# Kernel tuning notes

Hardware: AMD Instinct MI355X
Metric: run time of the kernel (lower is better)

## Reference

```python
import jax, jax.numpy as jnp
import numpy as np

NUM_HEADING_BIN = 12
NUM_SIZE_CLUSTER = 8
DELTA_NORM_W = 0.01
CENTER_W = 0.5
B, N = 4096, 2048


def huber(err, delta=1.0):
    a = jnp.abs(err)
    q = jnp.minimum(a, delta)
    return jnp.mean(0.5 * q * q + delta * (a - q))


def box3d_corners(centers, headings, sizes):
    # centers (B,3), headings (B,), sizes (B,3) -> (B,8,3)
    l, w, h = sizes[:, 0:1], sizes[:, 1:2], sizes[:, 2:3]
    sx = jnp.asarray([1, 1, -1, -1, 1, 1, -1, -1], dtype=sizes.dtype)
    sy = jnp.asarray([1, -1, -1, 1, 1, -1, -1, 1], dtype=sizes.dtype)
    sz = jnp.asarray([1, 1, 1, 1, -1, -1, -1, -1], dtype=sizes.dtype)
    corners = jnp.stack([0.5 * l * sx, 0.5 * w * sy, 0.5 * h * sz], axis=1)  # (B,3,8)
    c, s = jnp.cos(headings), jnp.sin(headings)
    z, o = jnp.zeros_like(c), jnp.ones_like(c)
    R = jnp.stack([jnp.stack([c, -s, z], -1),
                   jnp.stack([s, c, z], -1),
                   jnp.stack([z, z, o], -1)], axis=1)  # (B,3,3)
    out = jnp.einsum('bij,bjk->bik', R, corners) + centers[:, :, None]
    return jnp.transpose(out, (0, 2, 1))  # (B,8,3)


def setup_inputs() -> dict:
    key = jax.random.key(0)
    ks = jax.random.split(key, 9)
    return {
        'mask_xyz_mean': jax.random.normal(ks[0], (B, 3), jnp.float32),
        'point_cloud': jax.random.normal(ks[1], (B, 3, N), jnp.float32),
        'x_delta': jax.random.normal(ks[2], (B, 3, N), jnp.float32),
        'center_label': jax.random.normal(ks[3], (B, 3), jnp.float32),
        'size_residual_label': jax.random.normal(ks[4], (B, 3), jnp.float32),
        'heading_residual_label': jax.random.normal(ks[5], (B,), jnp.float32),
        'mean_sizes': jax.random.uniform(ks[6], (NUM_SIZE_CLUSTER, 3), jnp.float32, 0.5, 2.5),
        'size_class_label': jax.random.randint(ks[7], (B,), 0, NUM_SIZE_CLUSTER, jnp.int32),
        'heading_class_label': jax.random.randint(ks[8], (B,), 0, NUM_HEADING_BIN, jnp.int32),
    }


def reference(mask_xyz_mean, point_cloud, x_delta, center_label,
              size_residual_label, heading_residual_label, mean_sizes,
              size_class_label, heading_class_label):
    eps = 0.0  # faithful: original has no eps
    # center loss
    center_dist = jnp.linalg.norm(mask_xyz_mean - center_label, axis=1)
    center_loss = CENTER_W * huber(center_dist)

    # label assembly (onehot-sum == gather)
    size_label = mean_sizes[size_class_label] + size_residual_label  # (B,3)
    bin_centers = jnp.arange(0, np.pi, np.pi / NUM_HEADING_BIN, dtype=jnp.float32)
    heading_label = heading_residual_label + bin_centers[heading_class_label]  # (B,)

    corners_3d_gt = box3d_corners(center_label, heading_label, size_label)
    corners_2d_gt = corners_3d_gt[:, 4:8, :2]  # (B,4,2)

    v = center_label[:, :2]  # (B,2)
    p_dir = jnp.stack([-v[:, 1], v[:, 0]], axis=1)
    p_dir = p_dir / jnp.linalg.norm(p_dir, axis=1, keepdims=True)  # (B,2)

    pp_label = jnp.einsum('bkc,bc->bk', corners_2d_gt, p_dir)  # (B,4)
    py_max, py_min = jnp.max(pp_label, axis=1), jnp.min(pp_label, axis=1)
    std_y_label = (py_max - py_min) / 4
    mean_y_label = (py_max + py_min) / 2

    v_norm = jnp.linalg.norm(v, axis=1, keepdims=True)  # (B,1)
    proj_label = jnp.einsum('bkc,bc->bk', corners_2d_gt, v) / v_norm  # (B,4)
    p_max, p_min = jnp.max(proj_label, axis=1), jnp.min(proj_label, axis=1)
    std_label = (p_max - p_min) / 4
    mean_label = (p_max + p_min) / 2

    pc_xy = jnp.transpose(point_cloud, (0, 2, 1))[:, :, :2]  # (B,N,2)

    pp_pc = jnp.einsum('bnc,bc->bn', pc_xy, p_dir)  # (B,N)
    std_y_pc = jnp.std(pp_pc, axis=1, ddof=1)
    mean_y_pc = jnp.mean(pp_pc, axis=1)
    y_std_loss = huber(jnp.abs(std_y_label - std_y_pc))
    y_mean_loss = huber(jnp.abs(mean_y_label - mean_y_pc))

    proj_pc = jnp.einsum('bnc,bc->bn', pc_xy, v) / v_norm  # (B,N)
    std_pc = jnp.std(proj_pc, axis=1, ddof=1)
    mean_pc = jnp.mean(proj_pc, axis=1)
    x_std_loss = huber(jnp.abs(std_label - std_pc))
    x_mean_loss = huber(jnp.abs(mean_label - mean_pc))

    delta_norm = jnp.sqrt(jnp.sum(x_delta * x_delta, axis=(1, 2)))
    delta_norm_loss = DELTA_NORM_W * huber(delta_norm)

    total = center_loss + x_std_loss + x_mean_loss + delta_norm_loss + y_mean_loss + y_std_loss
    return 0.4 * total
```

## Files before the change

kernel.cpp:

```cpp
#include <hip/hip_runtime.h>
#include <math.h>

#define B_SZ 4096
#define N_PTS 2048
#define BLOCK 256

__device__ __forceinline__ float huber1(float a) {
    float q = fminf(a, 1.0f);
    return 0.5f * q * q + (a - q);
}

__global__ __launch_bounds__(BLOCK) void loss_stage1(
    const float* __restrict__ mask_xyz_mean,
    const float* __restrict__ point_cloud,
    const float* __restrict__ x_delta,
    const float* __restrict__ center_label,
    const float* __restrict__ size_residual,
    const float* __restrict__ heading_residual,
    const float* __restrict__ mean_sizes,
    const int*   __restrict__ size_class,
    const int*   __restrict__ heading_class,
    float* __restrict__ ws)
{
    const int b   = blockIdx.x;
    const int tid = threadIdx.x;

    const float cx = center_label[b * 3 + 0];
    const float cy = center_label[b * 3 + 1];

    const float vnorm2 = cx * cx + cy * cy;
    const float vnorm  = sqrtf(vnorm2);
    const float pdx = -cy / vnorm;
    const float pdy =  cx / vnorm;

    const size_t base = (size_t)b * 3 * N_PTS;
    const float4* px4 = (const float4*)(point_cloud + base);
    const float4* py4 = (const float4*)(point_cloud + base + N_PTS);
    const float4* pd4 = (const float4*)(x_delta + base);

    float s_pp = 0.f, s_pp2 = 0.f, s_t = 0.f, s_t2 = 0.f, s_d2 = 0.f;

    #pragma unroll
    for (int k = 0; k < N_PTS / 4 / BLOCK; ++k) {
        const int i = tid + k * BLOCK;
        const float4 x4 = px4[i];
        const float4 y4 = py4[i];
        {
            float pp = x4.x * pdx + y4.x * pdy;
            float t  = x4.x * cx  + y4.x * cy;
            s_pp += pp; s_pp2 += pp * pp; s_t += t; s_t2 += t * t;
        }
        {
            float pp = x4.y * pdx + y4.y * pdy;
            float t  = x4.y * cx  + y4.y * cy;
            s_pp += pp; s_pp2 += pp * pp; s_t += t; s_t2 += t * t;
        }
        {
            float pp = x4.z * pdx + y4.z * pdy;
            float t  = x4.z * cx  + y4.z * cy;
            s_pp += pp; s_pp2 += pp * pp; s_t += t; s_t2 += t * t;
        }
        {
            float pp = x4.w * pdx + y4.w * pdy;
            float t  = x4.w * cx  + y4.w * cy;
            s_pp += pp; s_pp2 += pp * pp; s_t += t; s_t2 += t * t;
        }
    }

    #pragma unroll
    for (int k = 0; k < 3 * N_PTS / 4 / BLOCK; ++k) {
        const int i = tid + k * BLOCK;
        const float4 d = pd4[i];
        s_d2 += d.x * d.x + d.y * d.y + d.z * d.z + d.w * d.w;
    }

    #pragma unroll
    for (int off = 32; off > 0; off >>= 1) {
        s_pp  += __shfl_down(s_pp,  off, 64);
        s_pp2 += __shfl_down(s_pp2, off, 64);
        s_t   += __shfl_down(s_t,   off, 64);
        s_t2  += __shfl_down(s_t2,  off, 64);
        s_d2  += __shfl_down(s_d2,  off, 64);
    }

    __shared__ float red[BLOCK / 64][5];
    const int wave = tid >> 6;
    const int lane = tid & 63;
    if (lane == 0) {
        red[wave][0] = s_pp;  red[wave][1] = s_pp2;
        red[wave][2] = s_t;   red[wave][3] = s_t2;
        red[wave][4] = s_d2;
    }
    __syncthreads();

    if (tid == 0) {
        #pragma unroll
        for (int w = 1; w < BLOCK / 64; ++w) {
            s_pp  += red[w][0];
            s_pp2 += red[w][1];
            s_t   += red[w][2];
            s_t2  += red[w][3];
            s_d2  += red[w][4];
        }

        const float mx = mask_xyz_mean[b * 3 + 0];
        const float my = mask_xyz_mean[b * 3 + 1];
        const float mz = mask_xyz_mean[b * 3 + 2];
        const float cz = center_label[b * 3 + 2];
        const float dxc = mx - cx, dyc = my - cy, dzc = mz - cz;
        const float center_dist = sqrtf(dxc * dxc + dyc * dyc + dzc * dzc);

        const int sc = size_class[b];
        const float l  = mean_sizes[sc * 3 + 0] + size_residual[b * 3 + 0];
        const float w_ = mean_sizes[sc * 3 + 1] + size_residual[b * 3 + 1];

        const float theta = heading_residual[b] +
                            (float)heading_class[b] * (float)(M_PI / 12.0);
        const float c = cosf(theta);
        const float s = sinf(theta);
        const float hl = 0.5f * l, hw = 0.5f * w_;

        float X[4], Y[4];
        X[0] =  c * hl - s * hw + cx;  Y[0] =  s * hl + c * hw + cy;
        X[1] =  c * hl + s * hw + cx;  Y[1] =  s * hl - c * hw + cy;
        X[2] = -c * hl + s * hw + cx;  Y[2] = -s * hl - c * hw + cy;
        X[3] = -c * hl - s * hw + cx;  Y[3] = -s * hl + c * hw + cy;

        float ppmax = -INFINITY, ppmin = INFINITY;
        float pmax  = -INFINITY, pmin  = INFINITY;
        #pragma unroll
        for (int k = 0; k < 4; ++k) {
            const float pp = X[k] * pdx + Y[k] * pdy;
            const float pj = (X[k] * cx + Y[k] * cy) / vnorm;
            ppmax = fmaxf(ppmax, pp); ppmin = fminf(ppmin, pp);
            pmax  = fmaxf(pmax,  pj); pmin  = fminf(pmin,  pj);
        }
        const float std_y_label  = (ppmax - ppmin) * 0.25f;
        const float mean_y_label = (ppmax + ppmin) * 0.5f;
        const float std_label    = (pmax - pmin) * 0.25f;
        const float mean_label   = (pmax + pmin) * 0.5f;

        const float invN   = 1.0f / (float)N_PTS;
        const float invNm1 = 1.0f / (float)(N_PTS - 1);

        const float mean_y_pc = s_pp * invN;
        const float var_y = (s_pp2 - s_pp * s_pp * invN) * invNm1;
        const float std_y_pc = sqrtf(fmaxf(var_y, 0.0f));

        const float mean_pc = (s_t * invN) / vnorm;
        const float var_x = ((s_t2 - s_t * s_t * invN) * invNm1) / vnorm2;
        const float std_pc = sqrtf(fmaxf(var_x, 0.0f));

        const float delta_norm = sqrtf(s_d2);

        const float total =
              0.5f  * huber1(center_dist)
            +         huber1(fabsf(std_label  - std_pc))
            +         huber1(fabsf(mean_label - mean_pc))
            + 0.01f * huber1(delta_norm)
            +         huber1(fabsf(mean_y_label - mean_y_pc))
            +         huber1(fabsf(std_y_label  - std_y_pc));

        ws[b] = total;
    }
}

__global__ __launch_bounds__(BLOCK) void loss_stage2(
    const float* __restrict__ ws, float* __restrict__ out)
{
    const int tid = threadIdx.x;
    const float4* w4 = (const float4*)ws;

    float s = 0.f;
    #pragma unroll
    for (int k = 0; k < B_SZ / 4 / BLOCK; ++k) {
        const float4 v = w4[tid + k * BLOCK];
        s += v.x + v.y + v.z + v.w;
    }

    #pragma unroll
    for (int off = 32; off > 0; off >>= 1)
        s += __shfl_down(s, off, 64);

    __shared__ float red[BLOCK / 64];
    const int wave = tid >> 6;
    const int lane = tid & 63;
    if (lane == 0) red[wave] = s;
    __syncthreads();

    if (tid == 0) {
        #pragma unroll
        for (int w = 1; w < BLOCK / 64; ++w) s += red[w];
        out[0] = s * (0.4f / (float)B_SZ);
    }
}

extern "C" void kernel_launch(void* const* d_in, const int* in_sizes, int n_in,
                              void* d_out, int out_size, void* d_ws, size_t ws_size,
                              hipStream_t stream) {
    const float* mask_xyz_mean    = (const float*)d_in[0];
    const float* point_cloud      = (const float*)d_in[1];
    const float* x_delta          = (const float*)d_in[2];
    const float* center_label     = (const float*)d_in[3];
    const float* size_residual    = (const float*)d_in[4];
    const float* heading_residual = (const float*)d_in[5];
    const float* mean_sizes       = (const float*)d_in[6];
    const int*   size_class       = (const int*)d_in[7];
    const int*   heading_class    = (const int*)d_in[8];
    float* ws  = (float*)d_ws;
    float* out = (float*)d_out;

    loss_stage1<<<B_SZ, BLOCK, 0, stream>>>(
        mask_xyz_mean, point_cloud, x_delta, center_label, size_residual,
        heading_residual, mean_sizes, size_class, heading_class, ws);
    loss_stage2<<<1, BLOCK, 0, stream>>>(ws, out);
}
```

Before: 221.6 us.

## Split per-batch reduction into two block roles and parallelize per-batch epilogue

Stage 1 now launches two blocks per batch element: one reduces point-cloud projections, the other reduces the squared norm of x_delta, so each block does less serial work. The scalar per-batch epilogue (sin/cos, corners, huber terms), which previously ran on a single thread per block, moves to a separate kernel that handles one batch element per thread. A third tiny kernel finishes the sum. This adds an extra kernel launch and more workspace traffic in exchange for more parallelism and less tail work per block.

After: 222.1 us. No clear change (+0.2%).

```diff
diff --git a/kernel.cpp b/kernel.cpp
--- a/kernel.cpp
+++ b/kernel.cpp
@@ -11,188 +11,208 @@
 }
 
 __global__ __launch_bounds__(BLOCK) void loss_stage1(
-    const float* __restrict__ mask_xyz_mean,
     const float* __restrict__ point_cloud,
     const float* __restrict__ x_delta,
+    const float* __restrict__ center_label,
+    float4* __restrict__ ws_pc,
+    float*  __restrict__ ws_d)
+{
+    const int b    = blockIdx.x >> 1;
+    const int role = blockIdx.x & 1;
+    const int tid  = threadIdx.x;
+    const int wave = tid >> 6;
+    const int lane = tid & 63;
+
+    const size_t base = (size_t)b * 3 * N_PTS;
+
+    __shared__ float red[BLOCK / 64][4];
+
+    if (role == 0) {
+        const float cx = center_label[b * 3 + 0];
+        const float cy = center_label[b * 3 + 1];
+        const float vnorm  = sqrtf(cx * cx + cy * cy);
+        const float pdx = -cy / vnorm;
+        const float pdy =  cx / vnorm;
+
+        const float4* px4 = (const float4*)(point_cloud + base);
+        const float4* py4 = (const float4*)(point_cloud + base + N_PTS);
+
+        const float4 x0 = px4[tid];
+        const float4 x1 = px4[tid + BLOCK];
+        const float4 y0 = py4[tid];
+        const float4 y1 = py4[tid + BLOCK];
+
+        float s_pp = 0.f, s_pp2 = 0.f, s_t = 0.f, s_t2 = 0.f;
+        const float xs[8] = {x0.x, x0.y, x0.z, x0.w, x1.x, x1.y, x1.z, x1.w};
+        const float ys[8] = {y0.x, y0.y, y0.z, y0.w, y1.x, y1.y, y1.z, y1.w};
+        #pragma unroll
+        for (int j = 0; j < 8; ++j) {
+            const float pp = xs[j] * pdx + ys[j] * pdy;
+            const float t  = xs[j] * cx  + ys[j] * cy;
+            s_pp += pp; s_pp2 += pp * pp; s_t += t; s_t2 += t * t;
+        }
+
+        #pragma unroll
+        for (int off = 32; off > 0; off >>= 1) {
+            s_pp  += __shfl_down(s_pp,  off, 64);
+            s_pp2 += __shfl_down(s_pp2, off, 64);
+            s_t   += __shfl_down(s_t,   off, 64);
+            s_t2  += __shfl_down(s_t2,  off, 64);
+        }
+        if (lane == 0) {
+            red[wave][0] = s_pp;  red[wave][1] = s_pp2;
+            red[wave][2] = s_t;   red[wave][3] = s_t2;
+        }
+        __syncthreads();
+        if (tid == 0) {
+            #pragma unroll
+            for (int w = 1; w < BLOCK / 64; ++w) {
+                s_pp  += red[w][0];
+                s_pp2 += red[w][1];
+                s_t   += red[w][2];
+                s_t2  += red[w][3];
+            }
+            ws_pc[b] = make_float4(s_pp, s_pp2, s_t, s_t2);
+        }
+    } else {
+        const float4* pd4 = (const float4*)(x_delta + base);
+
+        float4 d[6];
+        #pragma unroll
+        for (int k = 0; k < 6; ++k) d[k] = pd4[tid + k * BLOCK];
+
+        float a0 = 0.f, a1 = 0.f, a2 = 0.f, a3 = 0.f;
+        #pragma unroll
+        for (int k = 0; k < 6; ++k) {
+            a0 += d[k].x * d[k].x;
+            a1 += d[k].y * d[k].y;
+            a2 += d[k].z * d[k].z;
+            a3 += d[k].w * d[k].w;
+        }
+        float s_d2 = (a0 + a1) + (a2 + a3);
+
+        #pragma unroll
+        for (int off = 32; off > 0; off >>= 1)
+            s_d2 += __shfl_down(s_d2, off, 64);
+
+        if (lane == 0) red[wave][0] = s_d2;
+        __syncthreads();
+        if (tid == 0) {
+            #pragma unroll
+            for (int w = 1; w < BLOCK / 64; ++w) s_d2 += red[w][0];
+            ws_d[b] = s_d2;
+        }
+    }
+}
+
+__global__ __launch_bounds__(BLOCK) void loss_stage2(
+    const float4* __restrict__ ws_pc,
+    const float*  __restrict__ ws_d,
+    const float* __restrict__ mask_xyz_mean,
     const float* __restrict__ center_label,
     const float* __restrict__ size_residual,
     const float* __restrict__ heading_residual,
     const float* __restrict__ mean_sizes,
     const int*   __restrict__ size_class,
     const int*   __restrict__ heading_class,
-    float* __restrict__ ws)
+    float* __restrict__ ws_p)
 {
-    const int b   = blockIdx.x;
     const int tid = threadIdx.x;
+    const int b   = blockIdx.x * BLOCK + tid;
+
+    const float4 pcs = ws_pc[b];
+    const float s_pp = pcs.x, s_pp2 = pcs.y, s_t = pcs.z, s_t2 = pcs.w;
+    const float s_d2 = ws_d[b];
 
     const float cx = center_label[b * 3 + 0];
     const float cy = center_label[b * 3 + 1];
-
+    const float cz = center_label[b * 3 + 2];
     const float vnorm2 = cx * cx + cy * cy;
     const float vnorm  = sqrtf(vnorm2);
     const float pdx = -cy / vnorm;
     const float pdy =  cx / vnorm;
 
-    const size_t base = (size_t)b * 3 * N_PTS;
-    const float4* px4 = (const float4*)(point_cloud + base);
-    const float4* py4 = (const float4*)(point_cloud + base + N_PTS);
-    const float4* pd4 = (const float4*)(x_delta + base);
-
-    float s_pp = 0.f, s_pp2 = 0.f, s_t = 0.f, s_t2 = 0.f, s_d2 = 0.f;
-
+    const float mx = mask_xyz_mean[b * 3 + 0];
+    const float my = mask_xyz_mean[b * 3 + 1];
+    const float mz = mask_xyz_mean[b * 3 + 2];
+    const float dxc = mx - cx, dyc = my - cy, dzc = mz - cz;
+    const float center_dist = sqrtf(dxc * dxc + dyc * dyc + dzc * dzc);
+
+    const int sc = size_class[b];
+    const float l  = mean_sizes[sc * 3 + 0] + size_residual[b * 3 + 0];
+    const float w_ = mean_sizes[sc * 3 + 1] + size_residual[b * 3 + 1];
+
+    const float theta = heading_residual[b] +
+                        (float)heading_class[b] * (float)(M_PI / 12.0);
+    const float c = cosf(theta);
+    const float s = sinf(theta);
+    const float hl = 0.5f * l, hw = 0.5f * w_;
+
+    float X[4], Y[4];
+    X[0] =  c * hl - s * hw + cx;  Y[0] =  s * hl + c * hw + cy;
+    X[1] =  c * hl + s * hw + cx;  Y[1] =  s * hl - c * hw + cy;
+    X[2] = -c * hl + s * hw + cx;  Y[2] = -s * hl - c * hw + cy;
+    X[3] = -c * hl - s * hw + cx;  Y[3] = -s * hl + c * hw + cy;
+
+    float ppmax = -INFINITY, ppmin = INFINITY;
+    float pmax  = -INFINITY, pmin  = INFINITY;
     #pragma unroll
-    for (int k = 0; k < N_PTS / 4 / BLOCK; ++k) {
-        const int i = tid + k * BLOCK;
-        const float4 x4 = px4[i];
-        const float4 y4 = py4[i];
-        {
-            float pp = x4.x * pdx + y4.x * pdy;
-            float t  = x4.x * cx  + y4.x * cy;
-            s_pp += pp; s_pp2 += pp * pp; s_t += t; s_t2 += t * t;
-        }
-        {
-            float pp = x4.y * pdx + y4.y * pdy;
-            float t  = x4.y * cx  + y4.y * cy;
-            s_pp += pp; s_pp2 += pp * pp; s_t += t; s_t2 += t * t;
-        }
-        {
-            float pp = x4.z * pdx + y4.z * pdy;
-            float t  = x4.z * cx  + y4.z * cy;
-            s_pp += pp; s_pp2 += pp * pp; s_t += t; s_t2 += t * t;
-        }
-        {
-            float pp = x4.w * pdx + y4.w * pdy;
-            float t  = x4.w * cx  + y4.w * cy;
-            s_pp += pp; s_pp2 += pp * pp; s_t += t; s_t2 += t * t;
-        }
+    for (int k = 0; k < 4; ++k) {
+        const float pp = X[k] * pdx + Y[k] * pdy;
+        const float pj = (X[k] * cx + Y[k] * cy) / vnorm;
+        ppmax = fmaxf(ppmax, pp); ppmin = fminf(ppmin, pp);
+        pmax  = fmaxf(pmax,  pj); pmin  = fminf(pmin,  pj);
     }
+    const float std_y_label  = (ppmax - ppmin) * 0.25f;
+    const float mean_y_label = (ppmax + ppmin) * 0.5f;
+    const float std_label    = (pmax - pmin) * 0.25f;
+    const float mean_label   = (pmax + pmin) * 0.5f;
+
+    const float invN   = 1.0f / (float)N_PTS;
+    const float invNm1 = 1.0f / (float)(N_PTS - 1);
+
+    const float mean_y_pc = s_pp * invN;
+    const float var_y = (s_pp2 - s_pp * s_pp * invN) * invNm1;
+    const float std_y_pc = sqrtf(fmaxf(var_y, 0.0f));
+
+    const float mean_pc = (s_t * invN) / vnorm;
+    const float var_x = ((s_t2 - s_t * s_t * invN) * invNm1) / vnorm2;
+    const float std_pc = sqrtf(fmaxf(var_x, 0.0f));
+
+    const float delta_norm = sqrtf(s_d2);
+
+    float total =
+          0.5f  * huber1(center_dist)
+        +         huber1(fabsf(std_label  - std_pc))
+        +         huber1(fabsf(mean_label - mean_pc))
+        + 0.01f * huber1(delta_norm)
+        +         huber1(fabsf(mean_y_label - mean_y_pc))
+        +         huber1(fabsf(std_y_label  - std_y_pc));
 
     #pragma unroll
-    for (int k = 0; k < 3 * N_PTS / 4 / BLOCK; ++k) {
-        const int i = tid + k * BLOCK;
-        const float4 d = pd4[i];
-        s_d2 += d.x * d.x + d.y * d.y + d.z * d.z + d.w * d.w;
-    }
-
-    #pragma unroll
-    for (int off = 32; off > 0; off >>= 1) {
-        s_pp  += __shfl_down(s_pp,  off, 64);
-        s_pp2 += __shfl_down(s_pp2, off, 64);
-        s_t   += __shfl_down(s_t,   off, 64);
-        s_t2  += __shfl_down(s_t2,  off, 64);
-        s_d2  += __shfl_down(s_d2,  off, 64);
-    }
-
-    __shared__ float red[BLOCK / 64][5];
+    for (int off = 32; off > 0; off >>= 1)
+        total += __shfl_down(total, off, 64);
+
+    __shared__ float red[BLOCK / 64];
     const int wave = tid >> 6;
     const int lane = tid & 63;
-    if (lane == 0) {
-        red[wave][0] = s_pp;  red[wave][1] = s_pp2;
-        red[wave][2] = s_t;   red[wave][3] = s_t2;
-        red[wave][4] = s_d2;
+    if (lane == 0) red[wave] = total;
+    __syncthreads();
+    if (tid == 0) {
+        #pragma unroll
+        for (int w = 1; w < BLOCK / 64; ++w) total += red[w];
+        ws_p[blockIdx.x] = total;
     }
-    __syncthreads();
-
-    if (tid == 0) {
-        #pragma unroll
-        for (int w = 1; w < BLOCK / 64; ++w) {
-            s_pp  += red[w][0];
-            s_pp2 += red[w][1];
-            s_t   += red[w][2];
-            s_t2  += red[w][3];
-            s_d2  += red[w][4];
-        }
-
-        const float mx = mask_xyz_mean[b * 3 + 0];
-        const float my = mask_xyz_mean[b * 3 + 1];
-        const float mz = mask_xyz_mean[b * 3 + 2];
-        const float cz = center_label[b * 3 + 2];
-        const float dxc = mx - cx, dyc = my - cy, dzc = mz - cz;
-        const float center_dist = sqrtf(dxc * dxc + dyc * dyc + dzc * dzc);
-
-        const int sc = size_class[b];
-        const float l  = mean_sizes[sc * 3 + 0] + size_residual[b * 3 + 0];
-        const float w_ = mean_sizes[sc * 3 + 1] + size_residual[b * 3 + 1];
-
-        const float theta = heading_residual[b] +
-                            (float)heading_class[b] * (float)(M_PI / 12.0);
-        const float c = cosf(theta);
-        const float s = sinf(theta);
-        const float hl = 0.5f * l, hw = 0.5f * w_;
-
-        float X[4], Y[4];
-        X[0] =  c * hl - s * hw + cx;  Y[0] =  s * hl + c * hw + cy;
-        X[1] =  c * hl + s * hw + cx;  Y[1] =  s * hl - c * hw + cy;
-        X[2] = -c * hl + s * hw + cx;  Y[2] = -s * hl - c * hw + cy;
-        X[3] = -c * hl - s * hw + cx;  Y[3] = -s * hl + c * hw + cy;
-
-        float ppmax = -INFINITY, ppmin = INFINITY;
-        float pmax  = -INFINITY, pmin  = INFINITY;
-        #pragma unroll
-        for (int k = 0; k < 4; ++k) {
-            const float pp = X[k] * pdx + Y[k] * pdy;
-            const float pj = (X[k] * cx + Y[k] * cy) / vnorm;
-            ppmax = fmaxf(ppmax, pp); ppmin = fminf(ppmin, pp);
-            pmax  = fmaxf(pmax,  pj); pmin  = fminf(pmin,  pj);
-        }
-        const float std_y_label  = (ppmax - ppmin) * 0.25f;
-        const float mean_y_label = (ppmax + ppmin) * 0.5f;
-        const float std_label    = (pmax - pmin) * 0.25f;
-        const float mean_label   = (pmax + pmin) * 0.5f;
-
-        const float invN   = 1.0f / (float)N_PTS;
-        const float invNm1 = 1.0f / (float)(N_PTS - 1);
-
-        const float mean_y_pc = s_pp * invN;
-        const float var_y = (s_pp2 - s_pp * s_pp * invN) * invNm1;
-        const float std_y_pc = sqrtf(fmaxf(var_y, 0.0f));
-
-        const float mean_pc = (s_t * invN) / vnorm;
-        const float var_x = ((s_t2 - s_t * s_t * invN) * invNm1) / vnorm2;
-        const float std_pc = sqrtf(fmaxf(var_x, 0.0f));
-
-        const float delta_norm = sqrtf(s_d2);
-
-        const float total =
-              0.5f  * huber1(center_dist)
-            +         huber1(fabsf(std_label  - std_pc))
-            +         huber1(fabsf(mean_label - mean_pc))
-            + 0.01f * huber1(delta_norm)
-            +         huber1(fabsf(mean_y_label - mean_y_pc))
-            +         huber1(fabsf(std_y_label  - std_y_pc));
-
-        ws[b] = total;
-    }
-}
-
-__global__ __launch_bounds__(BLOCK) void loss_stage2(
-    const float* __restrict__ ws, float* __restrict__ out)
+}
+
+__global__ void loss_stage3(const float* __restrict__ ws_p, float* __restrict__ out)
 {
-    const int tid = threadIdx.x;
-    const float4* w4 = (const float4*)ws;
-
-    float s = 0.f;
-    #pragma unroll
-    for (int k = 0; k < B_SZ / 4 / BLOCK; ++k) {
-        const float4 v = w4[tid + k * BLOCK];
-        s += v.x + v.y + v.z + v.w;
-    }
-
+    const int lane = threadIdx.x;
+    float s = (lane < B_SZ / BLOCK) ? ws_p[lane] : 0.0f;
     #pragma unroll
     for (int off = 32; off > 0; off >>= 1)
         s += __shfl_down(s, off, 64);
-
-    __shared__ float red[BLOCK / 64];
-    const int wave = tid >> 6;
-    const int lane = tid & 63;
-    if (lane == 0) red[wave] = s;
-    __syncthreads();
-
-    if (tid == 0) {
-        #pragma unroll
-        for (int w = 1; w < BLOCK / 64; ++w) s += red[w];
-        out[0] = s * (0.4f / (float)B_SZ);
-    }
+    if (lane == 0) out[0] = s * (0.4f / (float)B_SZ);
 }
 
 extern "C" void kernel_launch(void* const* d_in, const int* in_sizes, int n_in,
@@ -207,11 +227,16 @@
     const float* mean_sizes       = (const float*)d_in[6];
     const int*   size_class       = (const int*)d_in[7];
     const int*   heading_class    = (const int*)d_in[8];
-    float* ws  = (float*)d_ws;
     float* out = (float*)d_out;
 
-    loss_stage1<<<B_SZ, BLOCK, 0, stream>>>(
-        mask_xyz_mean, point_cloud, x_delta, center_label, size_residual,
-        heading_residual, mean_sizes, size_class, heading_class, ws);
-    loss_stage2<<<1, BLOCK, 0, stream>>>(ws, out);
-}
+    float4* ws_pc = (float4*)d_ws;
+    float*  ws_d  = (float*)d_ws + B_SZ * 4;
+    float*  ws_p  = ws_d + B_SZ;
+
+    loss_stage1<<<2 * B_SZ, BLOCK, 0, stream>>>(
+        point_cloud, x_delta, center_label, ws_pc, ws_d);
+    loss_stage2<<<B_SZ / BLOCK, BLOCK, 0, stream>>>(
+        ws_pc, ws_d, mask_xyz_mean, center_label, size_residual,
+        heading_residual, mean_sizes, size_class, heading_class, ws_p);
+    loss_stage3<<<1, 64, 0, stream>>>(ws_p, out);
+}
```
